# Kernel optimization log

Hardware: AMD Instinct MI355X
Metric: run time of the kernel (lower is better)

## Reference

```python
import jax, jax.numpy as jnp
import numpy as np

LATENT = 3
HIDDEN = 16
INP = LATENT + 1  # prev_z cat action
B = 1048576


def setup_inputs() -> dict:
    key = jax.random.key(0)
    ks = jax.random.split(key, 11)
    s_ih = 1.0 / np.sqrt(HIDDEN)
    return {
        "prev_z": jax.random.normal(ks[0], (B, LATENT), jnp.float32),
        "action": jax.random.normal(ks[1], (B, 1), jnp.float32),
        "prev_h": jax.random.normal(ks[2], (B, HIDDEN), jnp.float32),
        # GRUCell params (torch layout: [3*H, in] and [3*H, H], gate order r,z,n)
        "W_ih": jax.random.uniform(ks[3], (3 * HIDDEN, INP), jnp.float32, -s_ih, s_ih),
        "W_hh": jax.random.uniform(ks[4], (3 * HIDDEN, HIDDEN), jnp.float32, -s_ih, s_ih),
        "b_ih": jax.random.uniform(ks[5], (3 * HIDDEN,), jnp.float32, -s_ih, s_ih),
        "b_hh": jax.random.uniform(ks[6], (3 * HIDDEN,), jnp.float32, -s_ih, s_ih),
        # prior heads
        "W_mu": jax.random.uniform(ks[7], (LATENT, HIDDEN), jnp.float32, -s_ih, s_ih),
        "b_mu": jax.random.uniform(ks[8], (LATENT,), jnp.float32, -s_ih, s_ih),
        "W_lv": jax.random.uniform(ks[9], (LATENT, HIDDEN), jnp.float32, -s_ih, s_ih),
        "b_lv": jax.random.uniform(ks[10], (LATENT,), jnp.float32, -s_ih, s_ih),
    }


def reference(prev_z, action, prev_h, W_ih, W_hh, b_ih, b_hh, W_mu, b_mu, W_lv, b_lv):
    x = jnp.concatenate([prev_z, action], axis=-1)              # [B, 4]
    gi = x @ W_ih.T + b_ih                                       # [B, 3H]
    gh = prev_h @ W_hh.T + b_hh                                  # [B, 3H]
    i_r, i_z, i_n = jnp.split(gi, 3, axis=-1)
    h_r, h_z, h_n = jnp.split(gh, 3, axis=-1)
    r = jax.nn.sigmoid(i_r + h_r)
    z = jax.nn.sigmoid(i_z + h_z)
    n = jnp.tanh(i_n + r * h_n)
    h = (1.0 - z) * n + z * prev_h                               # [B, H]
    mu = h @ W_mu.T + b_mu                                       # [B, 3]
    logvar = jnp.clip(h @ W_lv.T + b_lv, -5.0, 5.0)              # [B, 3]
    return mu, logvar, h
```

## Files before the change

### kernel.cpp

```cpp
#include <hip/hip_runtime.h>

#define TPB 256
#define WPT 4
#define ROW_DW 20
#define LDS_ROW_F32 (64 * ROW_DW)
#define LDS_MU_F32 192
#define LDS_WAVE_F32 (LDS_ROW_F32 + 2 * LDS_MU_F32)
#define LOG2E 1.44269504088896340736f

typedef _Float16 half8 __attribute__((ext_vector_type(8)));
typedef __fp16  fp16x2 __attribute__((ext_vector_type(2)));
typedef float f32x4 __attribute__((ext_vector_type(4)));

__device__ __forceinline__ half8 pack8(float4 lo, float4 hi) {
    union { fp16x2 p[4]; half8 h; } u;
    u.p[0] = __builtin_amdgcn_cvt_pkrtz(lo.x, lo.y);
    u.p[1] = __builtin_amdgcn_cvt_pkrtz(lo.z, lo.w);
    u.p[2] = __builtin_amdgcn_cvt_pkrtz(hi.x, hi.y);
    u.p[3] = __builtin_amdgcn_cvt_pkrtz(hi.z, hi.w);
    return u.h;
}


__global__ __launch_bounds__(64) void prep_kernel(
    const float* __restrict__ W_ih, const float* __restrict__ W_hh,
    const float* __restrict__ b_ih, const float* __restrict__ b_hh,
    const float* __restrict__ W_mu, const float* __restrict__ b_mu,
    const float* __restrict__ W_lv, const float* __restrict__ b_lv,
    void* __restrict__ wsv)
{
    _Float16* wsB = (_Float16*)wsv;
    const int l = threadIdx.x;
    const int col = l & 15, kg = l >> 4;

    #pragma unroll
    for (int t = 0; t < 4; ++t) {
        const int gate = (t == 0) ? col : (t == 1) ? (16 + col) : (32 + col);
        const float scale = (t <= 1) ? -LOG2E : -2.0f * LOG2E;
        #pragma unroll
        for (int i = 0; i < 8; ++i) {
            const int k = kg * 8 + i;
            float v = 0.f;
            if (t <= 1) {
                if (k < 4)       v = W_ih[gate * 4 + k];
                else if (k < 20) v = W_hh[gate * 16 + (k - 4)];
            } else if (t == 2) {
                if (k < 4)       v = W_ih[gate * 4 + k];
            } else {
                if (k >= 4 && k < 20) v = W_hh[gate * 16 + (k - 4)];
            }
            wsB[t * 512 + l * 8 + i] = (_Float16)(v * scale);
        }
    }
    #pragma unroll
    for (int i = 0; i < 8; ++i) {
        const int k = kg * 8 + i;
        wsB[4 * 512 + l * 8 + i] = (_Float16)((k == col + 4) ? 1.f : 0.f);
    }
    #pragma unroll
    for (int i = 0; i < 8; ++i) {
        const int k = kg * 8 + i;
        const int m = col;
        float v = 0.f;
        if (m < 3) {
            if (k < 16)       v = W_mu[m * 16 + k];
            else if (k == 20) v = b_mu[m];
        } else if (m < 6) {
            if (k < 16)       v = W_lv[(m - 3) * 16 + k];
            else if (k == 20) v = b_lv[m - 3];
        }
        wsB[5 * 512 + l * 8 + i] = (_Float16)v;
    }
    if (l < 16) {
        float4* b4 = (float4*)((char*)wsv + 6144);
        b4[l] = make_float4(-LOG2E * (b_ih[l] + b_hh[l]),
                            -LOG2E * (b_ih[16 + l] + b_hh[16 + l]),
                            -2.0f * LOG2E * b_ih[32 + l],
                            -2.0f * LOG2E * b_hh[32 + l]);
    }
}

template<bool EXACT>
__global__ __launch_bounds__(TPB, 6) void rssm_kernel(
    const float* __restrict__ prev_z,
    const float* __restrict__ action,
    const float* __restrict__ prev_h,
    const void*  __restrict__ wsv,
    float* __restrict__ out_mu,
    float* __restrict__ out_lv,
    float* __restrict__ out_h,
    int B)
{
    __shared__ float lds[4][LDS_WAVE_F32];
    const int tid = threadIdx.x;
    const int wid = tid >> 6, lane = tid & 63;
    const int col = lane & 15, kg = lane >> 4;
    const int wbase = (blockIdx.x * 4 + wid) * 64;
    if (!EXACT && wbase >= B) return;

    float* W  = lds[wid];
    float* MU = W + LDS_ROW_F32;
    float* LV = MU + LDS_MU_F32;

    const half8* Bp = (const half8*)wsv;
    const half8 bR  = Bp[lane];
    const half8 bZ  = Bp[64 + lane];
    const half8 bNi = Bp[128 + lane];
    const half8 bNh = Bp[192 + lane];
    const half8 bHp = Bp[256 + lane];
    const half8 a2  = Bp[320 + lane];
    const float4 bias = ((const float4*)((const char*)wsv + 6144))[col];

    {
        const float4* hg = (const float4*)prev_h;
        #pragma unroll
        for (int i = 0; i < 4; ++i) {
            const int fi = i * 64 + lane;
            const int r = fi >> 2, w = fi & 3;
            const int gi = EXACT ? (wbase * 4 + fi) : min(wbase * 4 + fi, B * 4 - 1);
            const float4 v = hg[gi];
            *(float4*)&W[r * ROW_DW + 4 + w * 4] = v;
        }
        const int zr = EXACT ? (wbase + lane) : min(wbase + lane, B - 1);
        const float z0 = prev_z[zr * 3 + 0];
        const float z1 = prev_z[zr * 3 + 1];
        const float z2 = prev_z[zr * 3 + 2];
        const float ac = action[zr];
        *(float4*)&W[lane * ROW_DW] = make_float4(z0, z1, z2, ac);
    }

    #pragma unroll
    for (int t = 0; t < WPT; ++t) {
        const float* ap = &W[(t * 16 + col) * ROW_DW + kg * 8];
        const float4 z4 = make_float4(0.f, 0.f, 0.f, 0.f);
        const float4 p0 = (kg < 3) ? *(const float4*)ap : z4;
        const float4 p1 = (kg < 2) ? *(const float4*)(ap + 4) : z4;
        const half8 a = pack8(p0, p1);

        f32x4 accR  = {bias.x, bias.x, bias.x, bias.x};
        f32x4 accZ  = {bias.y, bias.y, bias.y, bias.y};
        f32x4 accNi = {bias.z, bias.z, bias.z, bias.z};
        f32x4 accNh = {bias.w, bias.w, bias.w, bias.w};
        f32x4 accHp = {0.f, 0.f, 0.f, 0.f};
        accR  = __builtin_amdgcn_mfma_f32_16x16x32_f16(a, bR,  accR,  0, 0, 0);
        accZ  = __builtin_amdgcn_mfma_f32_16x16x32_f16(a, bZ,  accZ,  0, 0, 0);
        accNi = __builtin_amdgcn_mfma_f32_16x16x32_f16(a, bNi, accNi, 0, 0, 0);
        accNh = __builtin_amdgcn_mfma_f32_16x16x32_f16(a, bNh, accNh, 0, 0, 0);
        accHp = __builtin_amdgcn_mfma_f32_16x16x32_f16(a, bHp, accHp, 0, 0, 0);

        #pragma unroll
        for (int q = 0; q < 4; ++q) {
            const float r  = __builtin_amdgcn_rcpf(1.0f + __builtin_amdgcn_exp2f(accR[q]));
            const float z  = __builtin_amdgcn_rcpf(1.0f + __builtin_amdgcn_exp2f(accZ[q]));
            const float ta = fmaf(r, accNh[q], accNi[q]);
            const float n  = fmaf(2.0f,
                                  __builtin_amdgcn_rcpf(1.0f + __builtin_amdgcn_exp2f(ta)),
                                  -1.0f);
            const float hv = fmaf(z, accHp[q] - n, n);
            W[(t * 16 + kg * 4 + q) * ROW_DW + 4 + col] = hv;
        }

        half8 b2;
        if (kg < 2) {
            const float* hr = &W[(t * 16 + col) * ROW_DW + 4 + kg * 8];
            b2 = pack8(*(const float4*)hr, *(const float4*)(hr + 4));
        } else {
            #pragma unroll
            for (int i = 0; i < 8; ++i) b2[i] = (_Float16)0.f;
            if (kg == 2) b2[4] = (_Float16)1.0f;
        }
        f32x4 acc2 = {0.f, 0.f, 0.f, 0.f};
        acc2 = __builtin_amdgcn_mfma_f32_16x16x32_f16(a2, b2, acc2, 0, 0, 0);

        const int mr = (t * 16 + col) * 3;
        if (kg == 0) {
            MU[mr + 0] = acc2[0];
            MU[mr + 1] = acc2[1];
            MU[mr + 2] = acc2[2];
            LV[mr + 0] = fminf(fmaxf(acc2[3], -5.0f), 5.0f);
        } else if (kg == 1) {
            LV[mr + 1] = fminf(fmaxf(acc2[0], -5.0f), 5.0f);
            LV[mr + 2] = fminf(fmaxf(acc2[1], -5.0f), 5.0f);
        }

        {
            const int r = lane >> 2, w = lane & 3;
            const float4 hv4 = *(const float4*)&W[(t * 16 + r) * ROW_DW + 4 + w * 4];
            const int orow = wbase + t * 16 + r;
            if (EXACT || orow < B)
                *(float4*)&out_h[(size_t)orow * 16 + w * 4] = hv4;
        }
    }

    if (lane < 48) {
        const int gi = wbase * 3 + lane * 4;
        if (EXACT || gi + 3 < B * 3) {
            *(float4*)&out_mu[gi] = *(const float4*)&MU[lane * 4];
            *(float4*)&out_lv[gi] = *(const float4*)&LV[lane * 4];
        }
    }
}

extern "C" void kernel_launch(void* const* d_in, const int* in_sizes, int n_in,
                              void* d_out, int out_size, void* d_ws, size_t ws_size,
                              hipStream_t stream) {
    const float* prev_z = (const float*)d_in[0];
    const float* action = (const float*)d_in[1];
    const float* prev_h = (const float*)d_in[2];
    const float* W_ih   = (const float*)d_in[3];
    const float* W_hh   = (const float*)d_in[4];
    const float* b_ih   = (const float*)d_in[5];
    const float* b_hh   = (const float*)d_in[6];
    const float* W_mu   = (const float*)d_in[7];
    const float* b_mu   = (const float*)d_in[8];
    const float* W_lv   = (const float*)d_in[9];
    const float* b_lv   = (const float*)d_in[10];

    const int B = in_sizes[0] / 3;
    float* out    = (float*)d_out;
    float* out_mu = out;
    float* out_lv = out + (size_t)3 * B;
    float* out_h  = out + (size_t)6 * B;

    prep_kernel<<<1, 64, 0, stream>>>(W_ih, W_hh, b_ih, b_hh,
                                      W_mu, b_mu, W_lv, b_lv, d_ws);

    const int rows_per_block = 256;
    const int blocks = (B + rows_per_block - 1) / rows_per_block;
    if ((B % rows_per_block) == 0)
        rssm_kernel<true><<<blocks, TPB, 0, stream>>>(prev_z, action, prev_h, d_ws,
                                                      out_mu, out_lv, out_h, B);
    else
        rssm_kernel<false><<<blocks, TPB, 0, stream>>>(prev_z, action, prev_h, d_ws,
                                                       out_mu, out_lv, out_h, B);
}
```

Measured before the change: 41.52 us.

## Store staging rows in LDS as fp16 and halve block size

The per-wave LDS staging buffer now holds inputs and the new hidden state as fp16 instead of fp32. This removes repeated fp32-to-fp16 packing before each MFMA and halves LDS footprint. Blocks shrink from four waves to two, which may raise occupancy. The emitted h output is now rounded through fp16, which lowers its precision.

```diff
diff --git a/kernel.cpp b/kernel.cpp
--- a/kernel.cpp
+++ b/kernel.cpp
@@ -1,24 +1,27 @@
 #include <hip/hip_runtime.h>
 
-#define TPB 256
+#define TPB 128
 #define WPT 4
-#define ROW_DW 20
-#define LDS_ROW_F32 (64 * ROW_DW)
+#define ROW_H 36
+#define LDS_W_HALF (64 * ROW_H)
 #define LDS_MU_F32 192
-#define LDS_WAVE_F32 (LDS_ROW_F32 + 2 * LDS_MU_F32)
 #define LOG2E 1.44269504088896340736f
 
 typedef _Float16 half8 __attribute__((ext_vector_type(8)));
+typedef _Float16 half4 __attribute__((ext_vector_type(4)));
 typedef __fp16  fp16x2 __attribute__((ext_vector_type(2)));
 typedef float f32x4 __attribute__((ext_vector_type(4)));
 
-__device__ __forceinline__ half8 pack8(float4 lo, float4 hi) {
-    union { fp16x2 p[4]; half8 h; } u;
-    u.p[0] = __builtin_amdgcn_cvt_pkrtz(lo.x, lo.y);
-    u.p[1] = __builtin_amdgcn_cvt_pkrtz(lo.z, lo.w);
-    u.p[2] = __builtin_amdgcn_cvt_pkrtz(hi.x, hi.y);
-    u.p[3] = __builtin_amdgcn_cvt_pkrtz(hi.z, hi.w);
+__device__ __forceinline__ half4 cvt4(float4 v) {
+    union { fp16x2 p[2]; half4 h; } u;
+    u.p[0] = __builtin_amdgcn_cvt_pkrtz(v.x, v.y);
+    u.p[1] = __builtin_amdgcn_cvt_pkrtz(v.z, v.w);
     return u.h;
+}
+__device__ __forceinline__ half8 cat8(half4 a, half4 b) {
+    union { half4 q[2]; half8 o; } u;
+    u.q[0] = a; u.q[1] = b;
+    return u.o;
 }
 
 
@@ -91,16 +94,18 @@
     float* __restrict__ out_h,
     int B)
 {
-    __shared__ float lds[4][LDS_WAVE_F32];
+    __shared__ __align__(16) _Float16 Wl[2][LDS_W_HALF];
+    __shared__ float MUl[2][LDS_MU_F32];
+    __shared__ float LVl[2][LDS_MU_F32];
     const int tid = threadIdx.x;
     const int wid = tid >> 6, lane = tid & 63;
     const int col = lane & 15, kg = lane >> 4;
-    const int wbase = (blockIdx.x * 4 + wid) * 64;
+    const int wbase = (blockIdx.x * 2 + wid) * 64;
     if (!EXACT && wbase >= B) return;
 
-    float* W  = lds[wid];
-    float* MU = W + LDS_ROW_F32;
-    float* LV = MU + LDS_MU_F32;
+    _Float16* W = Wl[wid];
+    float* MU = MUl[wid];
+    float* LV = LVl[wid];
 
     const half8* Bp = (const half8*)wsv;
     const half8 bR  = Bp[lane];
@@ -112,30 +117,34 @@
     const float4 bias = ((const float4*)((const char*)wsv + 6144))[col];
 
     {
+        half4 z4h; z4h[0] = z4h[1] = z4h[2] = z4h[3] = (_Float16)0.f;
+        *(half4*)&W[lane * ROW_H + 20] = z4h;
+
         const float4* hg = (const float4*)prev_h;
         #pragma unroll
         for (int i = 0; i < 4; ++i) {
             const int fi = i * 64 + lane;
             const int r = fi >> 2, w = fi & 3;
             const int gi = EXACT ? (wbase * 4 + fi) : min(wbase * 4 + fi, B * 4 - 1);
-            const float4 v = hg[gi];
-            *(float4*)&W[r * ROW_DW + 4 + w * 4] = v;
+            *(half4*)&W[r * ROW_H + 4 + w * 4] = cvt4(hg[gi]);
         }
         const int zr = EXACT ? (wbase + lane) : min(wbase + lane, B - 1);
-        const float z0 = prev_z[zr * 3 + 0];
-        const float z1 = prev_z[zr * 3 + 1];
-        const float z2 = prev_z[zr * 3 + 2];
-        const float ac = action[zr];
-        *(float4*)&W[lane * ROW_DW] = make_float4(z0, z1, z2, ac);
+        *(half4*)&W[lane * ROW_H] =
+            cvt4(make_float4(prev_z[zr * 3 + 0], prev_z[zr * 3 + 1],
+                             prev_z[zr * 3 + 2], action[zr]));
     }
 
     #pragma unroll
     for (int t = 0; t < WPT; ++t) {
-        const float* ap = &W[(t * 16 + col) * ROW_DW + kg * 8];
-        const float4 z4 = make_float4(0.f, 0.f, 0.f, 0.f);
-        const float4 p0 = (kg < 3) ? *(const float4*)ap : z4;
-        const float4 p1 = (kg < 2) ? *(const float4*)(ap + 4) : z4;
-        const half8 a = pack8(p0, p1);
+        half8 a;
+        if (kg < 3) {
+            const half4 h0 = *(const half4*)&W[(t * 16 + col) * ROW_H + kg * 8];
+            const half4 h1 = *(const half4*)&W[(t * 16 + col) * ROW_H + kg * 8 + 4];
+            a = cat8(h0, h1);
+        } else {
+            half4 zz; zz[0] = zz[1] = zz[2] = zz[3] = (_Float16)0.f;
+            a = cat8(zz, zz);
+        }
 
         f32x4 accR  = {bias.x, bias.x, bias.x, bias.x};
         f32x4 accZ  = {bias.y, bias.y, bias.y, bias.y};
@@ -157,16 +166,17 @@
                                   __builtin_amdgcn_rcpf(1.0f + __builtin_amdgcn_exp2f(ta)),
                                   -1.0f);
             const float hv = fmaf(z, accHp[q] - n, n);
-            W[(t * 16 + kg * 4 + q) * ROW_DW + 4 + col] = hv;
+            W[(t * 16 + kg * 4 + q) * ROW_H + 4 + col] = (_Float16)hv;
         }
 
         half8 b2;
         if (kg < 2) {
-            const float* hr = &W[(t * 16 + col) * ROW_DW + 4 + kg * 8];
-            b2 = pack8(*(const float4*)hr, *(const float4*)(hr + 4));
+            const half4 b0 = *(const half4*)&W[(t * 16 + col) * ROW_H + 4 + kg * 8];
+            const half4 b1 = *(const half4*)&W[(t * 16 + col) * ROW_H + 8 + kg * 8];
+            b2 = cat8(b0, b1);
         } else {
-            #pragma unroll
-            for (int i = 0; i < 8; ++i) b2[i] = (_Float16)0.f;
+            half4 zz; zz[0] = zz[1] = zz[2] = zz[3] = (_Float16)0.f;
+            b2 = cat8(zz, zz);
             if (kg == 2) b2[4] = (_Float16)1.0f;
         }
         f32x4 acc2 = {0.f, 0.f, 0.f, 0.f};
@@ -185,7 +195,9 @@
 
         {
             const int r = lane >> 2, w = lane & 3;
-            const float4 hv4 = *(const float4*)&W[(t * 16 + r) * ROW_DW + 4 + w * 4];
+            const half4 hh = *(const half4*)&W[(t * 16 + r) * ROW_H + 4 + w * 4];
+            const float4 hv4 = make_float4((float)hh[0], (float)hh[1],
+                                           (float)hh[2], (float)hh[3]);
             const int orow = wbase + t * 16 + r;
             if (EXACT || orow < B)
                 *(float4*)&out_h[(size_t)orow * 16 + w * 4] = hv4;
@@ -225,7 +237,7 @@
     prep_kernel<<<1, 64, 0, stream>>>(W_ih, W_hh, b_ih, b_hh,
                                       W_mu, b_mu, W_lv, b_lv, d_ws);
 
-    const int rows_per_block = 256;
+    const int rows_per_block = 128;
     const int blocks = (B + rows_per_block - 1) / rows_per_block;
     if ((B % rows_per_block) == 0)
         rssm_kernel<true><<<blocks, TPB, 0, stream>>>(prev_z, action, prev_h, d_ws,
```

After: 42.29 us. No clear change (+1.8%).
